# Kernel optimization log

Measured on AMD Instinct MI355X. Metric: run time of the kernel, lower is better.

Reference implementation:

```python
import jax, jax.numpy as jnp
import numpy as np
from jax import lax

MAXV = 8      # convex intersection of two quads has at most 8 vertices
EPS = 1e-7
LOSS_WEIGHT = 1.0


def _edge_cross(A, B, P):
    # z of (B-A) x (P-A); >= 0 means P is on the left of directed edge A->B (inside for CCW poly)
    return (B[0] - A[0]) * (P[1] - A[1]) - (B[1] - A[1]) * (P[0] - A[0])


def _clip_halfplane(pts, n, A, B):
    # Sutherland-Hodgman clip of polygon pts[:n] against left halfplane of edge A->B.
    # pts: (MAXV,2) buffer, n: traced vertex count. Returns new buffer + count.
    def body(i, carry):
        out, m = carry
        valid = i < n
        cur = pts[i]
        nxt = pts[jnp.mod(i + 1, jnp.maximum(n, 1))]
        dc = _edge_cross(A, B, cur)
        dn = _edge_cross(A, B, nxt)
        denom = dc - dn
        t = dc / jnp.where(jnp.abs(denom) < EPS, 1.0, denom)
        ip = cur + t * (nxt - cur)
        add_cur = valid & (dc >= 0)
        idx = jnp.minimum(m, MAXV - 1)
        out = jnp.where(add_cur, out.at[idx].set(cur), out)
        m = m + add_cur.astype(jnp.int32)
        add_ip = valid & jnp.logical_xor(dc >= 0, dn >= 0)
        idx = jnp.minimum(m, MAXV - 1)
        out = jnp.where(add_ip, out.at[idx].set(ip), out)
        m = m + add_ip.astype(jnp.int32)
        return out, m
    out0 = jnp.zeros((MAXV, 2), pts.dtype)
    return lax.fori_loop(0, MAXV, body, (out0, jnp.int32(0)))


def _shoelace_masked(pts, n):
    # signed area of pts[:n] (fixed-size loop, masked)
    def body(i, acc):
        valid = i < n
        cur = pts[i]
        nxt = pts[jnp.mod(i + 1, jnp.maximum(n, 1))]
        term = cur[0] * nxt[1] - cur[1] * nxt[0]
        return acc + jnp.where(valid, term, jnp.zeros((), pts.dtype))
    return 0.5 * lax.fori_loop(0, MAXV, body, jnp.zeros((), pts.dtype))


def _quad_signed_area(p):  # p: (4,2)
    x, y = p[:, 0], p[:, 1]
    return 0.5 * jnp.sum(x * jnp.roll(y, -1) - y * jnp.roll(x, -1))


def _diou_single(p, t):
    # p, t: (4,2) quads -> scalar poly DIoU loss (a=0 => standard DIoU penalty)
    sa_p = _quad_signed_area(p)
    sa_t = _quad_signed_area(t)
    p = jnp.where(sa_p < 0, p[::-1], p)   # force CCW orientation
    t = jnp.where(sa_t < 0, t[::-1], t)
    area_p = jnp.abs(sa_p)
    area_t = jnp.abs(sa_t)
    # clip p by the 4 halfplanes of t
    buf = jnp.zeros((MAXV, 2), p.dtype).at[:4].set(p)
    n = jnp.int32(4)
    for k in range(4):
        buf, n = _clip_halfplane(buf, n, t[k], t[(k + 1) % 4])
    inter = jnp.abs(_shoelace_masked(buf, n))
    union = area_p + area_t - inter
    iou = inter / (union + EPS)
    cp = p.mean(0)
    ct = t.mean(0)
    d2 = jnp.sum((cp - ct) ** 2)
    allp = jnp.concatenate([p, t], axis=0)
    c2 = jnp.sum((allp.max(0) - allp.min(0)) ** 2) + EPS
    return 1.0 - iou + d2 / c2


def setup_inputs() -> dict:
    key = jax.random.key(0)
    k1, k2 = jax.random.split(key)
    N = 2_000_000
    pred = jax.random.uniform(k1, (N, 8), dtype=jnp.float32)
    target = jax.random.uniform(k2, (N, 8), dtype=jnp.float32)
    return {"pred": pred, "target": target}


def reference(pred, target):
    p = pred.reshape(-1, 4, 2)
    t = target.reshape(-1, 4, 2)
    losses = jax.vmap(_diou_single)(p, t)  # (N,)
    return LOSS_WEIGHT * losses.mean()
```

## Files before the change

### kernel.cpp

```cpp
#include <hip/hip_runtime.h>

#define NBLOCKS 2048
#define NTHREADS 256
#define FEPS 1e-7f

__device__ __forceinline__ float frcp(float x) { return __builtin_amdgcn_rcpf(x); }

__device__ __forceinline__ int clip1_to_lds(float2* base,
                                            const float (&px)[4], const float (&py)[4],
                                            float ex, float ey, float h) {
    float c[4];
#pragma unroll
    for (int j = 0; j < 4; ++j)
        c[j] = fmaf(ex, py[j], -fmaf(ey, px[j], h));
    int m = 0;
#pragma unroll
    for (int i = 0; i < 4; ++i) {
        const int ip1 = (i + 1) & 3;
        float dc = c[i], dn = c[ip1];
        float nx = px[ip1], ny = py[ip1];
        float denom = dc - dn;
        float d = (fabsf(denom) < FEPS) ? 1.0f : denom;
        float t = dc * frcp(d);
        float ipx = fmaf(t, nx - px[i], px[i]);
        float ipy = fmaf(t, ny - py[i], py[i]);
        bool sc = dc >= 0.0f, sn = dn >= 0.0f;

        bool add_cur = sc;
        int i1 = add_cur ? m : 8;
        base[i1 * NTHREADS] = make_float2(px[i], py[i]);
        m += add_cur;

        bool add_ip = (sc != sn);
        int i2 = add_ip ? m : 8;
        base[i2 * NTHREADS] = make_float2(ipx, ipy);
        m += add_ip;
    }
    return m;
}

__device__ __forceinline__ int clip_lds(float2* base, int n,
                                        float ex, float ey, float h) {
    float vx[8], vy[8], c[8];
#pragma unroll
    for (int j = 0; j < 8; ++j) {
        float2 v = base[j * NTHREADS];
        vx[j] = v.x; vy[j] = v.y;
        c[j] = fmaf(ex, vy[j], -fmaf(ey, vx[j], h));
    }
    int m = 0;
#pragma unroll
    for (int i = 0; i < 8; ++i) {
        if (i >= 4 && !__any(i < n)) break;
        bool valid = i < n;
        bool wrap = (i + 1 == n);
        const int ip1 = (i < 7) ? (i + 1) : 7;
        float nx = wrap ? vx[0] : vx[ip1];
        float ny = wrap ? vy[0] : vy[ip1];
        float dc = c[i];
        float dn = wrap ? c[0] : c[ip1];
        float denom = dc - dn;
        float d = (fabsf(denom) < FEPS) ? 1.0f : denom;
        float t = dc * frcp(d);
        float ipx = fmaf(t, nx - vx[i], vx[i]);
        float ipy = fmaf(t, ny - vy[i], vy[i]);
        bool sc = dc >= 0.0f, sn = dn >= 0.0f;

        bool add_cur = valid && sc;
        int i1;
        if (i < 4) i1 = add_cur ? m : 8;
        else       i1 = add_cur ? ((m < 7) ? m : 7) : 8;
        base[i1 * NTHREADS] = make_float2(vx[i], vy[i]);
        m += add_cur;

        bool add_ip = valid && (sc != sn);
        int i2;
        if (i < 4) i2 = add_ip ? m : 8;
        else       i2 = add_ip ? ((m < 7) ? m : 7) : 8;
        base[i2 * NTHREADS] = make_float2(ipx, ipy);
        m += add_ip;
    }
    return m;
}

__device__ __forceinline__ float diou_quad(float2* base,
                                           float4 pa, float4 pb, float4 ta, float4 tb) {
    float px[4] = {pa.x, pa.z, pb.x, pb.z};
    float py[4] = {pa.y, pa.w, pb.y, pb.w};
    float tx[4] = {ta.x, ta.z, tb.x, tb.z};
    float ty[4] = {ta.y, ta.w, tb.y, tb.w};

    float sa_p = 0.5f * ((px[0] * py[1] - py[0] * px[1]) +
                         (px[1] * py[2] - py[1] * px[2]) +
                         (px[2] * py[3] - py[2] * px[3]) +
                         (px[3] * py[0] - py[3] * px[0]));
    float sa_t = 0.5f * ((tx[0] * ty[1] - ty[0] * tx[1]) +
                         (tx[1] * ty[2] - ty[1] * tx[2]) +
                         (tx[2] * ty[3] - ty[2] * tx[3]) +
                         (tx[3] * ty[0] - ty[3] * tx[0]));

    if (sa_p < 0.0f) {
        float t0;
        t0 = px[0]; px[0] = px[3]; px[3] = t0;
        t0 = px[1]; px[1] = px[2]; px[2] = t0;
        t0 = py[0]; py[0] = py[3]; py[3] = t0;
        t0 = py[1]; py[1] = py[2]; py[2] = t0;
    }
    if (sa_t < 0.0f) {
        float t0;
        t0 = tx[0]; tx[0] = tx[3]; tx[3] = t0;
        t0 = tx[1]; tx[1] = tx[2]; tx[2] = t0;
        t0 = ty[0]; ty[0] = ty[3]; ty[3] = t0;
        t0 = ty[1]; ty[1] = ty[2]; ty[2] = t0;
    }
    float area_p = fabsf(sa_p);
    float area_t = fabsf(sa_t);

    int n;
    {
        float ex = tx[1] - tx[0], ey = ty[1] - ty[0];
        n = clip1_to_lds(base, px, py, ex, ey, fmaf(ex, ty[0], -ey * tx[0]));
    }
    {
        float ex = tx[2] - tx[1], ey = ty[2] - ty[1];
        n = clip_lds(base, n, ex, ey, fmaf(ex, ty[1], -ey * tx[1]));
    }
    {
        float ex = tx[3] - tx[2], ey = ty[3] - ty[2];
        n = clip_lds(base, n, ex, ey, fmaf(ex, ty[2], -ey * tx[2]));
    }
    {
        float ex = tx[0] - tx[3], ey = ty[0] - ty[3];
        n = clip_lds(base, n, ex, ey, fmaf(ex, ty[3], -ey * tx[3]));
    }

    float vx[8], vy[8];
#pragma unroll
    for (int j = 0; j < 8; ++j) {
        float2 v = base[j * NTHREADS];
        vx[j] = v.x; vy[j] = v.y;
    }
    float acc = 0.0f;
#pragma unroll
    for (int i = 0; i < 8; ++i) {
        if (i >= 4 && !__any(i < n)) break;
        bool valid = i < n;
        bool wrap = (i + 1 == n);
        const int ip1 = (i < 7) ? (i + 1) : 7;
        float nx = wrap ? vx[0] : vx[ip1];
        float ny = wrap ? vy[0] : vy[ip1];
        float term = vx[i] * ny - vy[i] * nx;
        acc += valid ? term : 0.0f;
    }
    float inter = fabsf(0.5f * acc);
    float uni = area_p + area_t - inter;
    float iou = inter * frcp(uni + FEPS);

    float cpx = 0.25f * (px[0] + px[1] + px[2] + px[3]);
    float cpy = 0.25f * (py[0] + py[1] + py[2] + py[3]);
    float ctx = 0.25f * (tx[0] + tx[1] + tx[2] + tx[3]);
    float cty = 0.25f * (ty[0] + ty[1] + ty[2] + ty[3]);
    float d2 = (cpx - ctx) * (cpx - ctx) + (cpy - cty) * (cpy - cty);

    float minx = fminf(fminf(fminf(px[0], px[1]), fminf(px[2], px[3])),
                       fminf(fminf(tx[0], tx[1]), fminf(tx[2], tx[3])));
    float maxx = fmaxf(fmaxf(fmaxf(px[0], px[1]), fmaxf(px[2], px[3])),
                       fmaxf(fmaxf(tx[0], tx[1]), fmaxf(tx[2], tx[3])));
    float miny = fminf(fminf(fminf(py[0], py[1]), fminf(py[2], py[3])),
                       fminf(fminf(ty[0], ty[1]), fminf(ty[2], ty[3])));
    float maxy = fmaxf(fmaxf(fmaxf(py[0], py[1]), fmaxf(py[2], py[3])),
                       fmaxf(fmaxf(ty[0], ty[1]), fmaxf(ty[2], ty[3])));
    float c2 = (maxx - minx) * (maxx - minx) + (maxy - miny) * (maxy - miny) + FEPS;

    return 1.0f - iou + d2 * frcp(c2);
}

__global__ __launch_bounds__(NTHREADS, 6) void diou_main(const float* __restrict__ pred,
                                                         const float* __restrict__ target,
                                                         double* __restrict__ partial,
                                                         int N) {
    __shared__ float2 poly[9 * NTHREADS];
    __shared__ double wsum[NTHREADS / 64];
    float2* base = &poly[threadIdx.x];

    const float4* p4 = reinterpret_cast<const float4*>(pred);
    const float4* t4 = reinterpret_cast<const float4*>(target);

    double acc = 0.0;
    for (int i = blockIdx.x * NTHREADS + threadIdx.x; i < N; i += NBLOCKS * NTHREADS) {
        float4 pa = p4[2 * i], pb = p4[2 * i + 1];
        float4 ta = t4[2 * i], tb = t4[2 * i + 1];
        acc += (double)diou_quad(base, pa, pb, ta, tb);
    }

#pragma unroll
    for (int off = 32; off > 0; off >>= 1) acc += __shfl_down(acc, off, 64);
    int lane = threadIdx.x & 63, wid = threadIdx.x >> 6;
    if (lane == 0) wsum[wid] = acc;
    __syncthreads();
    if (threadIdx.x == 0) {
        double s = 0.0;
#pragma unroll
        for (int w = 0; w < NTHREADS / 64; ++w) s += wsum[w];
        partial[blockIdx.x] = s;
    }
}

__global__ __launch_bounds__(256) void diou_finalize(const double* __restrict__ partial,
                                                     float* __restrict__ out,
                                                     int nparts, double invN) {
    __shared__ double s[256];
    double acc = 0.0;
    for (int i = threadIdx.x; i < nparts; i += 256) acc += partial[i];
    s[threadIdx.x] = acc;
    __syncthreads();
#pragma unroll
    for (int off = 128; off > 0; off >>= 1) {
        if (threadIdx.x < off) s[threadIdx.x] += s[threadIdx.x + off];
        __syncthreads();
    }
    if (threadIdx.x == 0) out[0] = (float)(s[0] * invN);
}

extern "C" void kernel_launch(void* const* d_in, const int* in_sizes, int n_in,
                              void* d_out, int out_size, void* d_ws, size_t ws_size,
                              hipStream_t stream) {
    const float* pred = (const float*)d_in[0];
    const float* target = (const float*)d_in[1];
    float* out = (float*)d_out;
    int N = in_sizes[0] / 8;

    double* partial = (double*)d_ws;

    diou_main<<<NBLOCKS, NTHREADS, 0, stream>>>(pred, target, partial, N);
    diou_finalize<<<1, 256, 0, stream>>>(partial, out, NBLOCKS, 1.0 / (double)N);
}
```

Baseline: 50.42 us.

## Vectorize vertex math with packed float2 ops and prefetch next iteration loads

Rewrites the per-vertex geometry in 2-wide float vectors so the compiler can emit packed FP32 instructions (v_pk_fma/mul/add on CDNA3). It also software-pipelines the grid-stride loop by loading the next element's pred/target before computing the current one, and raises the launch-bounds occupancy hint from 6 to 8 waves. The prefetch hides global load latency but adds live registers, which the tighter occupancy bound may force into spills.

```diff
diff --git a/kernel.cpp b/kernel.cpp
--- a/kernel.cpp
+++ b/kernel.cpp
@@ -4,49 +4,55 @@
 #define NTHREADS 256
 #define FEPS 1e-7f
 
+typedef __attribute__((ext_vector_type(2))) float f32x2;
+
 __device__ __forceinline__ float frcp(float x) { return __builtin_amdgcn_rcpf(x); }
 
-__device__ __forceinline__ int clip1_to_lds(float2* base,
-                                            const float (&px)[4], const float (&py)[4],
+__device__ __forceinline__ float cross2(f32x2 a, f32x2 b) {
+    f32x2 bs = __builtin_shufflevector(b, b, 1, 0);
+    f32x2 m = a * bs;
+    return m.x - m.y;
+}
+
+__device__ __forceinline__ int clip1_to_lds(f32x2* base, const f32x2 (&p)[4],
                                             float ex, float ey, float h) {
     float c[4];
 #pragma unroll
     for (int j = 0; j < 4; ++j)
-        c[j] = fmaf(ex, py[j], -fmaf(ey, px[j], h));
+        c[j] = fmaf(ex, p[j].y, -fmaf(ey, p[j].x, h));
     int m = 0;
 #pragma unroll
     for (int i = 0; i < 4; ++i) {
         const int ip1 = (i + 1) & 3;
         float dc = c[i], dn = c[ip1];
-        float nx = px[ip1], ny = py[ip1];
+        f32x2 cur = p[i], nxt = p[ip1];
         float denom = dc - dn;
         float d = (fabsf(denom) < FEPS) ? 1.0f : denom;
         float t = dc * frcp(d);
-        float ipx = fmaf(t, nx - px[i], px[i]);
-        float ipy = fmaf(t, ny - py[i], py[i]);
+        f32x2 ts = {t, t};
+        f32x2 ip = __builtin_elementwise_fma(ts, nxt - cur, cur);
         bool sc = dc >= 0.0f, sn = dn >= 0.0f;
 
-        bool add_cur = sc;
-        int i1 = add_cur ? m : 8;
-        base[i1 * NTHREADS] = make_float2(px[i], py[i]);
-        m += add_cur;
-
-        bool add_ip = (sc != sn);
-        int i2 = add_ip ? m : 8;
-        base[i2 * NTHREADS] = make_float2(ipx, ipy);
-        m += add_ip;
+        int i1 = sc ? m : 8;
+        base[i1 * NTHREADS] = cur;
+        m += sc;
+
+        bool aip = (sc != sn);
+        int i2 = aip ? m : 8;
+        base[i2 * NTHREADS] = ip;
+        m += aip;
     }
     return m;
 }
 
-__device__ __forceinline__ int clip_lds(float2* base, int n,
+__device__ __forceinline__ int clip_lds(f32x2* base, int n,
                                         float ex, float ey, float h) {
-    float vx[8], vy[8], c[8];
+    f32x2 v[8];
+    float c[8];
 #pragma unroll
     for (int j = 0; j < 8; ++j) {
-        float2 v = base[j * NTHREADS];
-        vx[j] = v.x; vy[j] = v.y;
-        c[j] = fmaf(ex, vy[j], -fmaf(ey, vx[j], h));
+        v[j] = base[j * NTHREADS];
+        c[j] = fmaf(ex, v[j].y, -fmaf(ey, v[j].x, h));
     }
     int m = 0;
 #pragma unroll
@@ -55,91 +61,78 @@
         bool valid = i < n;
         bool wrap = (i + 1 == n);
         const int ip1 = (i < 7) ? (i + 1) : 7;
-        float nx = wrap ? vx[0] : vx[ip1];
-        float ny = wrap ? vy[0] : vy[ip1];
+        f32x2 nxt = wrap ? v[0] : v[ip1];
         float dc = c[i];
         float dn = wrap ? c[0] : c[ip1];
+        f32x2 cur = v[i];
         float denom = dc - dn;
         float d = (fabsf(denom) < FEPS) ? 1.0f : denom;
         float t = dc * frcp(d);
-        float ipx = fmaf(t, nx - vx[i], vx[i]);
-        float ipy = fmaf(t, ny - vy[i], vy[i]);
+        f32x2 ts = {t, t};
+        f32x2 ip = __builtin_elementwise_fma(ts, nxt - cur, cur);
         bool sc = dc >= 0.0f, sn = dn >= 0.0f;
 
         bool add_cur = valid && sc;
         int i1;
         if (i < 4) i1 = add_cur ? m : 8;
         else       i1 = add_cur ? ((m < 7) ? m : 7) : 8;
-        base[i1 * NTHREADS] = make_float2(vx[i], vy[i]);
+        base[i1 * NTHREADS] = cur;
         m += add_cur;
 
         bool add_ip = valid && (sc != sn);
         int i2;
         if (i < 4) i2 = add_ip ? m : 8;
         else       i2 = add_ip ? ((m < 7) ? m : 7) : 8;
-        base[i2 * NTHREADS] = make_float2(ipx, ipy);
+        base[i2 * NTHREADS] = ip;
         m += add_ip;
     }
     return m;
 }
 
-__device__ __forceinline__ float diou_quad(float2* base,
-                                           float4 pa, float4 pb, float4 ta, float4 tb) {
-    float px[4] = {pa.x, pa.z, pb.x, pb.z};
-    float py[4] = {pa.y, pa.w, pb.y, pb.w};
-    float tx[4] = {ta.x, ta.z, tb.x, tb.z};
-    float ty[4] = {ta.y, ta.w, tb.y, tb.w};
-
-    float sa_p = 0.5f * ((px[0] * py[1] - py[0] * px[1]) +
-                         (px[1] * py[2] - py[1] * px[2]) +
-                         (px[2] * py[3] - py[2] * px[3]) +
-                         (px[3] * py[0] - py[3] * px[0]));
-    float sa_t = 0.5f * ((tx[0] * ty[1] - ty[0] * tx[1]) +
-                         (tx[1] * ty[2] - ty[1] * tx[2]) +
-                         (tx[2] * ty[3] - ty[2] * tx[3]) +
-                         (tx[3] * ty[0] - ty[3] * tx[0]));
+__device__ __forceinline__ float diou_quad(f32x2* base,
+                                           float4 Pa, float4 Pb, float4 Ta, float4 Tb) {
+    f32x2 p[4] = {{Pa.x, Pa.y}, {Pa.z, Pa.w}, {Pb.x, Pb.y}, {Pb.z, Pb.w}};
+    f32x2 t[4] = {{Ta.x, Ta.y}, {Ta.z, Ta.w}, {Tb.x, Tb.y}, {Tb.z, Tb.w}};
+
+    float sa_p = 0.5f * (cross2(p[0], p[1]) + cross2(p[1], p[2]) +
+                         cross2(p[2], p[3]) + cross2(p[3], p[0]));
+    float sa_t = 0.5f * (cross2(t[0], t[1]) + cross2(t[1], t[2]) +
+                         cross2(t[2], t[3]) + cross2(t[3], t[0]));
 
     if (sa_p < 0.0f) {
-        float t0;
-        t0 = px[0]; px[0] = px[3]; px[3] = t0;
-        t0 = px[1]; px[1] = px[2]; px[2] = t0;
-        t0 = py[0]; py[0] = py[3]; py[3] = t0;
-        t0 = py[1]; py[1] = py[2]; py[2] = t0;
+        f32x2 w;
+        w = p[0]; p[0] = p[3]; p[3] = w;
+        w = p[1]; p[1] = p[2]; p[2] = w;
     }
     if (sa_t < 0.0f) {
-        float t0;
-        t0 = tx[0]; tx[0] = tx[3]; tx[3] = t0;
-        t0 = tx[1]; tx[1] = tx[2]; tx[2] = t0;
-        t0 = ty[0]; ty[0] = ty[3]; ty[3] = t0;
-        t0 = ty[1]; ty[1] = ty[2]; ty[2] = t0;
+        f32x2 w;
+        w = t[0]; t[0] = t[3]; t[3] = w;
+        w = t[1]; t[1] = t[2]; t[2] = w;
     }
     float area_p = fabsf(sa_p);
     float area_t = fabsf(sa_t);
 
     int n;
     {
-        float ex = tx[1] - tx[0], ey = ty[1] - ty[0];
-        n = clip1_to_lds(base, px, py, ex, ey, fmaf(ex, ty[0], -ey * tx[0]));
-    }
-    {
-        float ex = tx[2] - tx[1], ey = ty[2] - ty[1];
-        n = clip_lds(base, n, ex, ey, fmaf(ex, ty[1], -ey * tx[1]));
-    }
-    {
-        float ex = tx[3] - tx[2], ey = ty[3] - ty[2];
-        n = clip_lds(base, n, ex, ey, fmaf(ex, ty[2], -ey * tx[2]));
-    }
-    {
-        float ex = tx[0] - tx[3], ey = ty[0] - ty[3];
-        n = clip_lds(base, n, ex, ey, fmaf(ex, ty[3], -ey * tx[3]));
-    }
-
-    float vx[8], vy[8];
-#pragma unroll
-    for (int j = 0; j < 8; ++j) {
-        float2 v = base[j * NTHREADS];
-        vx[j] = v.x; vy[j] = v.y;
-    }
+        float ex = t[1].x - t[0].x, ey = t[1].y - t[0].y;
+        n = clip1_to_lds(base, p, ex, ey, fmaf(ex, t[0].y, -ey * t[0].x));
+    }
+    {
+        float ex = t[2].x - t[1].x, ey = t[2].y - t[1].y;
+        n = clip_lds(base, n, ex, ey, fmaf(ex, t[1].y, -ey * t[1].x));
+    }
+    {
+        float ex = t[3].x - t[2].x, ey = t[3].y - t[2].y;
+        n = clip_lds(base, n, ex, ey, fmaf(ex, t[2].y, -ey * t[2].x));
+    }
+    {
+        float ex = t[0].x - t[3].x, ey = t[0].y - t[3].y;
+        n = clip_lds(base, n, ex, ey, fmaf(ex, t[3].y, -ey * t[3].x));
+    }
+
+    f32x2 v[8];
+#pragma unroll
+    for (int j = 0; j < 8; ++j) v[j] = base[j * NTHREADS];
     float acc = 0.0f;
 #pragma unroll
     for (int i = 0; i < 8; ++i) {
@@ -147,50 +140,67 @@
         bool valid = i < n;
         bool wrap = (i + 1 == n);
         const int ip1 = (i < 7) ? (i + 1) : 7;
-        float nx = wrap ? vx[0] : vx[ip1];
-        float ny = wrap ? vy[0] : vy[ip1];
-        float term = vx[i] * ny - vy[i] * nx;
+        f32x2 nxt = wrap ? v[0] : v[ip1];
+        float term = cross2(v[i], nxt);
         acc += valid ? term : 0.0f;
     }
     float inter = fabsf(0.5f * acc);
     float uni = area_p + area_t - inter;
     float iou = inter * frcp(uni + FEPS);
 
-    float cpx = 0.25f * (px[0] + px[1] + px[2] + px[3]);
-    float cpy = 0.25f * (py[0] + py[1] + py[2] + py[3]);
-    float ctx = 0.25f * (tx[0] + tx[1] + tx[2] + tx[3]);
-    float cty = 0.25f * (ty[0] + ty[1] + ty[2] + ty[3]);
-    float d2 = (cpx - ctx) * (cpx - ctx) + (cpy - cty) * (cpy - cty);
-
-    float minx = fminf(fminf(fminf(px[0], px[1]), fminf(px[2], px[3])),
-                       fminf(fminf(tx[0], tx[1]), fminf(tx[2], tx[3])));
-    float maxx = fmaxf(fmaxf(fmaxf(px[0], px[1]), fmaxf(px[2], px[3])),
-                       fmaxf(fmaxf(tx[0], tx[1]), fmaxf(tx[2], tx[3])));
-    float miny = fminf(fminf(fminf(py[0], py[1]), fminf(py[2], py[3])),
-                       fminf(fminf(ty[0], ty[1]), fminf(ty[2], ty[3])));
-    float maxy = fmaxf(fmaxf(fmaxf(py[0], py[1]), fmaxf(py[2], py[3])),
-                       fmaxf(fmaxf(ty[0], ty[1]), fmaxf(ty[2], ty[3])));
-    float c2 = (maxx - minx) * (maxx - minx) + (maxy - miny) * (maxy - miny) + FEPS;
+    f32x2 cp = (p[0] + p[1] + p[2] + p[3]) * 0.25f;
+    f32x2 ct = (t[0] + t[1] + t[2] + t[3]) * 0.25f;
+    f32x2 e = cp - ct;
+    f32x2 e2 = e * e;
+    float d2 = e2.x + e2.y;
+
+    f32x2 mn = __builtin_elementwise_min(
+        __builtin_elementwise_min(__builtin_elementwise_min(p[0], p[1]),
+                                  __builtin_elementwise_min(p[2], p[3])),
+        __builtin_elementwise_min(__builtin_elementwise_min(t[0], t[1]),
+                                  __builtin_elementwise_min(t[2], t[3])));
+    f32x2 mx = __builtin_elementwise_max(
+        __builtin_elementwise_max(__builtin_elementwise_max(p[0], p[1]),
+                                  __builtin_elementwise_max(p[2], p[3])),
+        __builtin_elementwise_max(__builtin_elementwise_max(t[0], t[1]),
+                                  __builtin_elementwise_max(t[2], t[3])));
+    f32x2 dd = mx - mn;
+    f32x2 dd2 = dd * dd;
+    float c2 = dd2.x + dd2.y + FEPS;
 
     return 1.0f - iou + d2 * frcp(c2);
 }
 
-__global__ __launch_bounds__(NTHREADS, 6) void diou_main(const float* __restrict__ pred,
+__global__ __launch_bounds__(NTHREADS, 8) void diou_main(const float* __restrict__ pred,
                                                          const float* __restrict__ target,
                                                          double* __restrict__ partial,
                                                          int N) {
-    __shared__ float2 poly[9 * NTHREADS];
+    __shared__ f32x2 poly[9 * NTHREADS];
     __shared__ double wsum[NTHREADS / 64];
-    float2* base = &poly[threadIdx.x];
+    f32x2* base = &poly[threadIdx.x];
 
     const float4* p4 = reinterpret_cast<const float4*>(pred);
     const float4* t4 = reinterpret_cast<const float4*>(target);
 
+    const int stride = NBLOCKS * NTHREADS;
+    int i = blockIdx.x * NTHREADS + threadIdx.x;
     double acc = 0.0;
-    for (int i = blockIdx.x * NTHREADS + threadIdx.x; i < N; i += NBLOCKS * NTHREADS) {
+    if (i < N) {
         float4 pa = p4[2 * i], pb = p4[2 * i + 1];
         float4 ta = t4[2 * i], tb = t4[2 * i + 1];
-        acc += (double)diou_quad(base, pa, pb, ta, tb);
+        for (;;) {
+            int inx = i + stride;
+            bool has = inx < N;
+            float4 npa, npb, nta, ntb;
+            if (has) {
+                npa = p4[2 * inx]; npb = p4[2 * inx + 1];
+                nta = t4[2 * inx]; ntb = t4[2 * inx + 1];
+            }
+            acc += (double)diou_quad(base, pa, pb, ta, tb);
+            if (!has) break;
+            pa = npa; pb = npb; ta = nta; tb = ntb;
+            i = inx;
+        }
     }
 
 #pragma unroll
```

Measured after the change: 64.97 us. 1.29x slower.
